# Kernel optimization log

Hardware: AMD Instinct MI355X
Metric: run time of the kernel (lower is better)

Reference implementation:

```python
import jax, jax.numpy as jnp
import numpy as np

CHUNK = 128
EPS = 1e-12


def causal_prod(q, k, v, chunk=CHUNK):
    """Chunk-parallel causal linear attention numerator and denominator.
    q,k: [B,H,S,D]; v: [B,H,S,E].
    Returns N: [B,H,S,E] = q_n . cumsum_{m<=n}(k_m v_m^T)
            D: [B,H,S]   = q_n . cumsum_{m<=n} k_m
    """
    B, H, S, D = q.shape
    E = v.shape[-1]
    nc = S // chunk
    # [nc, B, H, C, D]
    qc = q.reshape(B, H, nc, chunk, D).transpose(2, 0, 1, 3, 4)
    kc = k.reshape(B, H, nc, chunk, D).transpose(2, 0, 1, 3, 4)
    vc = v.reshape(B, H, nc, chunk, E).transpose(2, 0, 1, 3, 4)
    mask = jnp.tril(jnp.ones((chunk, chunk), dtype=bool))  # j <= i

    def step(carry, xs):
        S_state, Z_state = carry  # [B,H,D,E], [B,H,D]
        qb, kb, vb = xs           # [B,H,C,D], [B,H,C,D], [B,H,C,E]
        scores = jnp.einsum('bhid,bhjd->bhij', qb, kb)
        scores = jnp.where(mask, scores, 0.0)
        # intra-chunk causal part + inter-chunk state part
        Nb = jnp.einsum('bhij,bhje->bhie', scores, vb) \
             + jnp.einsum('bhid,bhde->bhie', qb, S_state)
        Db = scores.sum(-1) + jnp.einsum('bhid,bhd->bhi', qb, Z_state)
        S_state = S_state + jnp.einsum('bhjd,bhje->bhde', kb, vb)
        Z_state = Z_state + kb.sum(axis=2)
        return (S_state, Z_state), (Nb, Db)

    init = (jnp.zeros((B, H, D, E), q.dtype), jnp.zeros((B, H, D), q.dtype))
    _, (N, Dv) = jax.lax.scan(step, init, (qc, kc, vc))
    N = N.transpose(1, 2, 0, 3, 4).reshape(B, H, S, E)
    Dv = Dv.transpose(1, 2, 0, 3).reshape(B, H, S)
    return N, Dv


def setup_inputs() -> dict:
    key = jax.random.key(0)
    k0, k1, k2, k3, k4 = jax.random.split(key, 5)
    B, H, S, D = 2, 8, 4096, 64
    # feature-mapped q/k are positive (softmax random features) -> uniform
    q = jax.random.uniform(k0, (B, H, S, D), dtype=jnp.float32)
    k = jax.random.uniform(k1, (B, H, S, D), dtype=jnp.float32)
    q_rot = jax.random.uniform(k2, (B, H, S, D), dtype=jnp.float32)
    k_rot = jax.random.uniform(k3, (B, H, S, D), dtype=jnp.float32)
    v = jax.random.normal(k4, (B, H, S, D), dtype=jnp.float32)
    return {"q": q, "k": k, "q_rot": q_rot, "k_rot": k_rot, "v": v, "horizon": 512}


def reference(q, k, q_rot, k_rot, v, horizon):
    # causal_linear_attention with local=horizon, rotary branch active
    N1, D1 = causal_prod(q, k, v)
    N2, D2 = causal_prod(q_rot, k_rot, v)
    N = N1 + N2
    Dd = D1 + D2
    local = horizon
    # subtract contribution of keys older than the local window
    ql = q[:, :, local:]
    kl = k[:, :, :-local]
    vl = v[:, :, :-local]
    qrl = q_rot[:, :, local:]
    krl = k_rot[:, :, :-local]
    Ns1, Ds1 = causal_prod(ql, kl, vl)
    Ns2, Ds2 = causal_prod(qrl, krl, vl)
    N = N.at[:, :, local:].add(-(Ns1 + Ns2))
    Dd = Dd.at[:, :, local:].add(-(Ds1 + Ds2))
    out = N * (1.0 / (Dd + EPS))[..., None]
    return out
```

## Files before the change

kernel.cpp:

```cpp
#include <hip/hip_runtime.h>

#define S_LEN 4096
#define Dh 64
#define KC_TILE 16384
#define VT_TILE 8192

typedef __attribute__((ext_vector_type(8))) short bf16x8;
typedef __attribute__((ext_vector_type(4))) short bf16x4;
typedef __attribute__((ext_vector_type(4))) float f32x4;
typedef __attribute__((ext_vector_type(16))) float f32x16;
typedef __attribute__((ext_vector_type(4))) unsigned u32x4;

__device__ __forceinline__ short f2bf(float f) {
    union { float f; unsigned u; } c; c.f = f;
    unsigned u = c.u + 0x7FFFu + ((c.u >> 16) & 1u);
    return (short)(u >> 16);
}

__device__ __forceinline__ unsigned cvt_pk(float lo, float hi) {
    unsigned r;
    asm("v_cvt_pk_bf16_f32 %0, %1, %2" : "=v"(r) : "v"(lo), "v"(hi));
    return r;
}

__device__ __forceinline__ void pl32swap(unsigned& a, unsigned& b) {
    asm("v_permlane32_swap_b32 %0, %1" : "+v"(a), "+v"(b));
}

__global__ __launch_bounds__(256) void prepack2(
    const float* __restrict__ k, const float* __restrict__ kr,
    const float* __restrict__ v, char* __restrict__ ws,
    unsigned long long vt_base, int k_slots)
{
    const int t = blockIdx.x * 256 + threadIdx.x;
    if (t < k_slots) {
        const int bh = t >> 16;
        const int r = t & 65535;
        const int tile = r >> 10;
        const int s = r & 1023;
        const int l = s & 63;
        const int c = s >> 6;
        const int fs = c >> 1, half = c & 1;
        const int key = half * 32 + (l & 31);
        const int f0 = fs * 16 + (l >> 5) * 8;
        const size_t row = ((size_t)bh * S_LEN + tile * 64 + key) * Dh;
        const float* src = (f0 < 64) ? (k + row + f0) : (kr + row + f0 - 64);
        f32x4 a = *(const f32x4*)src;
        f32x4 b = *(const f32x4*)(src + 4);
        u32x4 w;
        w[0] = cvt_pk(a[0], a[1]); w[1] = cvt_pk(a[2], a[3]);
        w[2] = cvt_pk(b[0], b[1]); w[3] = cvt_pk(b[2], b[3]);
        *(u32x4*)(ws + (size_t)(bh * 64 + tile) * KC_TILE + s * 16) = w;
    } else {
        const int t2 = t - k_slots;
        const int bh = t2 >> 15;
        const int r = t2 & 32767;
        const int tile = r >> 9;
        const int s = r & 511;
        const int l = s & 63;
        const int c = s >> 6;
        const int kb = c >> 2, ks = (c >> 1) & 1, eh = c & 1;
        const int e = eh * 32 + (l & 31);
        const int key0 = kb * 32 + ks * 16 + (l >> 5) * 8;
        const float* src = v + ((size_t)bh * S_LEN + tile * 64 + key0) * Dh + e;
        float x0 = src[0],      x1 = src[Dh],     x2 = src[2 * Dh], x3 = src[3 * Dh];
        float x4 = src[4 * Dh], x5 = src[5 * Dh], x6 = src[6 * Dh], x7 = src[7 * Dh];
        u32x4 w;
        w[0] = cvt_pk(x0, x1); w[1] = cvt_pk(x2, x3);
        w[2] = cvt_pk(x4, x5); w[3] = cvt_pk(x6, x7);
        *(u32x4*)(ws + vt_base + (size_t)(bh * 64 + tile) * VT_TILE + s * 16) = w;
    }
}

__global__ __launch_bounds__(64, 2) void swin_attn4(
    const float* __restrict__ q, const float* __restrict__ qr,
    const char* __restrict__ ws, unsigned long long vt_base,
    const int* __restrict__ hor, float* __restrict__ out)
{
    const int W = hor[0];
    const int nwg = gridDim.x;
    const int cpx = nwg >> 3;
    const int bid = blockIdx.x;
    const int wg = (bid & 7) * cpx + (bid >> 3);
    const int bh = wg >> 7;
    const int q0 = (wg & 127) * 32;
    const size_t base = (size_t)bh * S_LEN * Dh;

    const int lane = threadIdx.x;
    const int hi = lane >> 5;
    const int l32 = lane & 31;

    __shared__ float sD[32];

    const int qg = q0 + l32;

    bf16x8 qf[8];
    {
        const float* qrow  = q  + base + (size_t)qg * Dh;
        const float* qrrow = qr + base + (size_t)qg * Dh;
        #pragma unroll
        for (int fs = 0; fs < 8; ++fs) {
            int feat = fs * 16 + hi * 8;
            const float* src = (feat < 64) ? (qrow + feat) : (qrrow + feat - 64);
            f32x4 a = *(const f32x4*)src;
            f32x4 b = *(const f32x4*)(src + 4);
            u32x4 w;
            w[0] = cvt_pk(a[0], a[1]); w[1] = cvt_pk(a[2], a[3]);
            w[2] = cvt_pk(b[0], b[1]); w[3] = cvt_pk(b[2], b[3]);
            qf[fs] = __builtin_bit_cast(bf16x8, w);
        }
    }

    f32x16 nacc0 = {};
    f32x16 nacc1 = {};
    float dsum = 0.f;

    const int lo_key = q0 - (W - 1);
    const int kt_lo = (lo_key <= 0) ? 0 : (lo_key >> 6);
    const int kt_hi = (q0 + 31) >> 6;

    const char* Kc = ws + (size_t)(bh << 6) * KC_TILE + lane * 16;
    const char* Vt = ws + vt_base + (size_t)(bh << 6) * VT_TILE + lane * 16;

    bf16x8 kf[16];
    bf16x8 vf[8];
    {
        const char* kp = Kc + (size_t)kt_lo * KC_TILE;
        const char* vp = Vt + (size_t)kt_lo * VT_TILE;
        #pragma unroll
        for (int c = 0; c < 16; ++c) kf[c] = *(const bf16x8*)(kp + c * 1024);
        #pragma unroll
        for (int c = 0; c < 8; ++c)  vf[c] = *(const bf16x8*)(vp + c * 1024);
    }

    for (int kt = kt_lo; kt <= kt_hi; ++kt) {
        const int k0 = kt << 6;
        const int ktn = (kt < kt_hi) ? kt + 1 : kt_hi;
        const bool dense = (k0 + 63 <= q0) && (k0 >= q0 + 32 - W);

        f32x16 sac0 = {};
        f32x16 sac1 = {};
        __builtin_amdgcn_s_setprio(1);
        #pragma unroll
        for (int fs = 0; fs < 8; ++fs) {
            sac0 = __builtin_amdgcn_mfma_f32_32x32x16_bf16(kf[fs * 2],     qf[fs], sac0, 0, 0, 0);
            sac1 = __builtin_amdgcn_mfma_f32_32x32x16_bf16(kf[fs * 2 + 1], qf[fs], sac1, 0, 0, 0);
        }
        __builtin_amdgcn_s_setprio(0);

        {
            const char* kp = Kc + (size_t)ktn * KC_TILE;
            #pragma unroll
            for (int c = 0; c < 16; ++c) kf[c] = *(const bf16x8*)(kp + c * 1024);
        }

        #pragma unroll
        for (int kb = 0; kb < 2; ++kb) {
            f32x16 s = kb ? sac1 : sac0;
            if (!dense) {
                #pragma unroll
                for (int r = 0; r < 16; ++r) {
                    int key = k0 + kb * 32 + (r & 3) + 8 * (r >> 2) + 4 * hi;
                    if ((unsigned)(qg - key) >= (unsigned)W) s[r] = 0.f;
                }
            }
            #pragma unroll
            for (int r = 0; r < 16; ++r) dsum += s[r];

            unsigned w0 = cvt_pk(s[0],  s[1]);
            unsigned w1 = cvt_pk(s[2],  s[3]);
            unsigned w2 = cvt_pk(s[4],  s[5]);
            unsigned w3 = cvt_pk(s[6],  s[7]);
            unsigned w4 = cvt_pk(s[8],  s[9]);
            unsigned w5 = cvt_pk(s[10], s[11]);
            unsigned w6 = cvt_pk(s[12], s[13]);
            unsigned w7 = cvt_pk(s[14], s[15]);
            pl32swap(w0, w2);
            pl32swap(w1, w3);
            pl32swap(w4, w6);
            pl32swap(w5, w7);
            u32x4 p0v = {w0, w1, w2, w3};
            u32x4 p1v = {w4, w5, w6, w7};
            bf16x8 pa0 = __builtin_bit_cast(bf16x8, p0v);
            bf16x8 pa1 = __builtin_bit_cast(bf16x8, p1v);

            __builtin_amdgcn_s_setprio(1);
            #pragma unroll
            for (int ks = 0; ks < 2; ++ks) {
                bf16x8 pa = ks ? pa1 : pa0;
                nacc0 = __builtin_amdgcn_mfma_f32_32x32x16_bf16(pa, vf[kb * 4 + ks * 2],     nacc0, 0, 0, 0);
                nacc1 = __builtin_amdgcn_mfma_f32_32x32x16_bf16(pa, vf[kb * 4 + ks * 2 + 1], nacc1, 0, 0, 0);
            }
            __builtin_amdgcn_s_setprio(0);
        }

        {
            const char* vp = Vt + (size_t)ktn * VT_TILE;
            #pragma unroll
            for (int c = 0; c < 8; ++c) vf[c] = *(const bf16x8*)(vp + c * 1024);
        }
    }

    unsigned da = __builtin_bit_cast(unsigned, dsum);
    unsigned db = da;
    pl32swap(da, db);
    float dfull = __builtin_bit_cast(float, da) + __builtin_bit_cast(float, db);
    float rcq = 1.0f / (dfull + 1e-12f);
    if (lane < 32) sD[l32] = rcq;
    __syncthreads();
    float rcv[16];
    #pragma unroll
    for (int r = 0; r < 16; ++r)
        rcv[r] = sD[(r & 3) + 8 * (r >> 2) + 4 * hi];

    #pragma unroll
    for (int r = 0; r < 16; ++r) {
        const int qrow = q0 + (r & 3) + 8 * (r >> 2) + 4 * hi;
        float* o = out + base + (size_t)qrow * Dh + l32;
        o[0]  = nacc0[r] * rcv[r];
        o[32] = nacc1[r] * rcv[r];
    }
}

__global__ __launch_bounds__(256, 2) void swin_attn_fb(
    const float* __restrict__ q, const float* __restrict__ k,
    const float* __restrict__ qr, const float* __restrict__ kr,
    const float* __restrict__ v, const int* __restrict__ hor,
    float* __restrict__ out)
{
    const int W = hor[0];
    const int q0 = blockIdx.x * 128;
    const int bh = blockIdx.y;
    const size_t base = (size_t)bh * S_LEN * Dh;

    const int tid = threadIdx.x;
    const int lane = tid & 63;
    const int wv = tid >> 6;
    const int g = lane >> 4;
    const int l16 = lane & 15;

    __shared__ __align__(16) char sK[64 * 256];
    __shared__ __align__(16) char sV[64 * 128];
    __shared__ __align__(16) char sS[4][32 * 128];

    bf16x8 qf[2][4];
    #pragma unroll
    for (int rb = 0; rb < 2; ++rb) {
        int qg = q0 + wv * 32 + rb * 16 + l16;
        const float* qrow  = q  + base + (size_t)qg * Dh;
        const float* qrrow = qr + base + (size_t)qg * Dh;
        #pragma unroll
        for (int fb = 0; fb < 4; ++fb) {
            int feat = fb * 32 + g * 8;
            const float* src = (feat < 64) ? (qrow + feat) : (qrrow + (feat - 64));
            f32x4 a = *(const f32x4*)src;
            f32x4 b = *(const f32x4*)(src + 4);
            bf16x8 fr;
            #pragma unroll
            for (int j = 0; j < 4; ++j) { fr[j] = f2bf(a[j]); fr[4 + j] = f2bf(b[j]); }
            qf[rb][fb] = fr;
        }
    }

    f32x4 nacc[2][4];
    f32x4 dacc[2];
    #pragma unroll
    for (int rb = 0; rb < 2; ++rb) {
        dacc[rb] = (f32x4){0.f, 0.f, 0.f, 0.f};
        #pragma unroll
        for (int eb = 0; eb < 4; ++eb) nacc[rb][eb] = (f32x4){0.f, 0.f, 0.f, 0.f};
    }
    bf16x8 ones;
    #pragma unroll
    for (int j = 0; j < 8; ++j) ones[j] = (short)0x3F80;

    const int lo_key = q0 - (W - 1);
    const int kt_lo = (lo_key <= 0) ? 0 : (lo_key >> 6);
    const int kt_hi = (q0 + 127) >> 6;

    for (int kt = kt_lo; kt <= kt_hi; ++kt) {
        const int k0 = kt << 6;
        __syncthreads();
        #pragma unroll
        for (int i = 0; i < 4; ++i) {
            int c = tid + 256 * i;
            int row = c >> 4;
            int f0 = (c & 15) * 8;
            const float* src = (f0 < 64) ? (k  + base + (size_t)(k0 + row) * Dh + f0)
                                         : (kr + base + (size_t)(k0 + row) * Dh + (f0 - 64));
            f32x4 a = *(const f32x4*)src;
            f32x4 b = *(const f32x4*)(src + 4);
            bf16x8 w8;
            #pragma unroll
            for (int j = 0; j < 4; ++j) { w8[j] = f2bf(a[j]); w8[4 + j] = f2bf(b[j]); }
            int off = row * 256 + ((f0 * 2) ^ ((row & 7) << 4));
            *(bf16x8*)(sK + off) = w8;
        }
        #pragma unroll
        for (int i = 0; i < 4; ++i) {
            int c = tid + 256 * i;
            int e = c & 63;
            int k4 = c >> 6;
            const float* src = v + base + (size_t)(k0 + k4 * 4) * Dh + e;
            bf16x4 w4;
            w4[0] = f2bf(src[0]); w4[1] = f2bf(src[Dh]);
            w4[2] = f2bf(src[2 * Dh]); w4[3] = f2bf(src[3 * Dh]);
            int off = e * 128 + ((k4 * 8) ^ ((e & 7) << 4));
            *(bf16x4*)(sV + off) = w4;
        }
        __syncthreads();

        const bool dense = (k0 + 63 <= q0) && (k0 >= q0 + 128 - W);
        #pragma unroll
        for (int kb = 0; kb < 4; ++kb) {
            bf16x8 kf[4];
            const int key = kb * 16 + l16;
            const int rowoff = key * 256;
            const int sw = (key & 7) << 4;
            #pragma unroll
            for (int fb = 0; fb < 4; ++fb)
                kf[fb] = *(const bf16x8*)(sK + rowoff + ((fb * 64 + g * 16) ^ sw));
            #pragma unroll
            for (int rb = 0; rb < 2; ++rb) {
                f32x4 s = {0.f, 0.f, 0.f, 0.f};
                #pragma unroll
                for (int fb = 0; fb < 4; ++fb)
                    s = __builtin_amdgcn_mfma_f32_16x16x32_bf16(qf[rb][fb], kf[fb], s, 0, 0, 0);
                const int qrow0 = rb * 16 + g * 4;
                const int qg0 = q0 + wv * 32 + qrow0;
                const int mg = k0 + kb * 16 + l16;
                if (!dense) {
                    #pragma unroll
                    for (int r = 0; r < 4; ++r) {
                        unsigned d = (unsigned)(qg0 + r - mg);
                        if (d >= (unsigned)W) s[r] = 0.f;
                    }
                }
                #pragma unroll
                for (int r = 0; r < 4; ++r) {
                    int row = qrow0 + r;
                    int off = row * 128 + (((kb * 16 + l16) * 2) ^ ((row & 7) << 4));
                    *(short*)(sS[wv] + off) = f2bf(s[r]);
                }
            }
        }
        #pragma unroll
        for (int kb2 = 0; kb2 < 2; ++kb2) {
            bf16x8 af[2];
            #pragma unroll
            for (int rb = 0; rb < 2; ++rb) {
                int row = rb * 16 + l16;
                int off = row * 128 + ((kb2 * 64 + g * 16) ^ ((row & 7) << 4));
                af[rb] = *(const bf16x8*)(sS[wv] + off);
            }
            #pragma unroll
            for (int rb = 0; rb < 2; ++rb)
                dacc[rb] = __builtin_amdgcn_mfma_f32_16x16x32_bf16(af[rb], ones, dacc[rb], 0, 0, 0);
            #pragma unroll
            for (int eb = 0; eb < 4; ++eb) {
                int e = eb * 16 + l16;
                int off = e * 128 + ((kb2 * 64 + g * 16) ^ ((e & 7) << 4));
                bf16x8 bfr = *(const bf16x8*)(sV + off);
                #pragma unroll
                for (int rb = 0; rb < 2; ++rb)
                    nacc[rb][eb] = __builtin_amdgcn_mfma_f32_16x16x32_bf16(af[rb], bfr, nacc[rb][eb], 0, 0, 0);
            }
        }
    }

    #pragma unroll
    for (int rb = 0; rb < 2; ++rb) {
        f32x4 rc;
        #pragma unroll
        for (int r = 0; r < 4; ++r) rc[r] = 1.0f / (dacc[rb][r] + 1e-12f);
        const int qg0 = q0 + wv * 32 + rb * 16 + g * 4;
        #pragma unroll
        for (int eb = 0; eb < 4; ++eb) {
            #pragma unroll
            for (int r = 0; r < 4; ++r) {
                out[base + (size_t)(qg0 + r) * Dh + eb * 16 + l16] = nacc[rb][eb][r] * rc[r];
            }
        }
    }
}

extern "C" void kernel_launch(void* const* d_in, const int* in_sizes, int n_in,
                              void* d_out, int out_size, void* d_ws, size_t ws_size,
                              hipStream_t stream) {
    const float* q  = (const float*)d_in[0];
    const float* k  = (const float*)d_in[1];
    const float* qr = (const float*)d_in[2];
    const float* kr = (const float*)d_in[3];
    const float* v  = (const float*)d_in[4];
    const int* hor  = (const int*)d_in[5];
    float* out = (float*)d_out;

    const int BH = in_sizes[0] / (S_LEN * Dh);
    const unsigned long long vt_base = (unsigned long long)BH * 64 * KC_TILE;
    const unsigned long long ws_need = (unsigned long long)BH * 64 * (KC_TILE + VT_TILE);
    const int k_slots = BH * 65536;

    if (ws_size >= ws_need) {
        const int total_slots = BH * (65536 + 32768);
        hipLaunchKernelGGL(prepack2, dim3(total_slots / 256), dim3(256), 0, stream,
                           k, kr, v, (char*)d_ws, vt_base, k_slots);
        hipLaunchKernelGGL(swin_attn4, dim3(BH * 128), dim3(64), 0, stream,
                           q, qr, (const char*)d_ws, vt_base, hor, out);
    } else {
        hipLaunchKernelGGL(swin_attn_fb, dim3(S_LEN / 128, BH), dim3(256), 0, stream,
                           q, k, qr, kr, v, hor, out);
    }
}
```

Measured before the change: 42.31 us.

## Iterate key tiles at 32-key granularity to trim window edges and registers

The key loop now walks half-tiles of 32 keys instead of 64, so the windowed range starts and ends tighter around each 32-query block and skips partly empty half-tiles at the edges. The smaller prefetched K/V register arrays lower register pressure, and launch bounds are raised to allow three waves per SIMD. In exchange there are more loop iterations, each with its own masking, bf16 conversion and lane-swap overhead, and less MFMA work per iteration for hiding prefetch latency.

```diff
diff --git a/kernel.cpp b/kernel.cpp
--- a/kernel.cpp
+++ b/kernel.cpp
@@ -72,7 +72,7 @@
     }
 }
 
-__global__ __launch_bounds__(64, 2) void swin_attn4(
+__global__ __launch_bounds__(64, 3) void swin_attn5(
     const float* __restrict__ q, const float* __restrict__ qr,
     const char* __restrict__ ws, unsigned long long vt_base,
     const int* __restrict__ hor, float* __restrict__ out)
@@ -115,91 +115,77 @@
     f32x16 nacc1 = {};
     float dsum = 0.f;
 
-    const int lo_key = q0 - (W - 1);
-    const int kt_lo = (lo_key <= 0) ? 0 : (lo_key >> 6);
-    const int kt_hi = (q0 + 31) >> 6;
+    const int lo_q = q0 - W + 1;
+    const int h_lo = (lo_q <= 0) ? 0 : (lo_q >> 5);
+    const int h_hi = (q0 + 31) >> 5;
 
     const char* Kc = ws + (size_t)(bh << 6) * KC_TILE + lane * 16;
     const char* Vt = ws + vt_base + (size_t)(bh << 6) * VT_TILE + lane * 16;
 
-    bf16x8 kf[16];
-    bf16x8 vf[8];
-    {
-        const char* kp = Kc + (size_t)kt_lo * KC_TILE;
-        const char* vp = Vt + (size_t)kt_lo * VT_TILE;
-        #pragma unroll
-        for (int c = 0; c < 16; ++c) kf[c] = *(const bf16x8*)(kp + c * 1024);
-        #pragma unroll
-        for (int c = 0; c < 8; ++c)  vf[c] = *(const bf16x8*)(vp + c * 1024);
-    }
-
-    for (int kt = kt_lo; kt <= kt_hi; ++kt) {
-        const int k0 = kt << 6;
-        const int ktn = (kt < kt_hi) ? kt + 1 : kt_hi;
-        const bool dense = (k0 + 63 <= q0) && (k0 >= q0 + 32 - W);
-
-        f32x16 sac0 = {};
-        f32x16 sac1 = {};
+#define KADDR(H, FS) (Kc + (size_t)((H) >> 1) * KC_TILE + ((((FS) << 1) + ((H) & 1)) << 10))
+#define VADDR(H, C)  (Vt + (size_t)((H) >> 1) * VT_TILE + (((((H) & 1) << 2) + (C)) << 10))
+
+    bf16x8 kf[8];
+    bf16x8 vf[4];
+    #pragma unroll
+    for (int fs = 0; fs < 8; ++fs) kf[fs] = *(const bf16x8*)KADDR(h_lo, fs);
+    #pragma unroll
+    for (int c = 0; c < 4; ++c)    vf[c] = *(const bf16x8*)VADDR(h_lo, c);
+
+    for (int h = h_lo; h <= h_hi; ++h) {
+        const int hn = (h < h_hi) ? h + 1 : h;
+        const int k0h = h << 5;
+
+        f32x16 sac = {};
         __builtin_amdgcn_s_setprio(1);
         #pragma unroll
-        for (int fs = 0; fs < 8; ++fs) {
-            sac0 = __builtin_amdgcn_mfma_f32_32x32x16_bf16(kf[fs * 2],     qf[fs], sac0, 0, 0, 0);
-            sac1 = __builtin_amdgcn_mfma_f32_32x32x16_bf16(kf[fs * 2 + 1], qf[fs], sac1, 0, 0, 0);
-        }
+        for (int fs = 0; fs < 8; ++fs)
+            sac = __builtin_amdgcn_mfma_f32_32x32x16_bf16(kf[fs], qf[fs], sac, 0, 0, 0);
         __builtin_amdgcn_s_setprio(0);
 
-        {
-            const char* kp = Kc + (size_t)ktn * KC_TILE;
-            #pragma unroll
-            for (int c = 0; c < 16; ++c) kf[c] = *(const bf16x8*)(kp + c * 1024);
-        }
-
-        #pragma unroll
-        for (int kb = 0; kb < 2; ++kb) {
-            f32x16 s = kb ? sac1 : sac0;
-            if (!dense) {
-                #pragma unroll
-                for (int r = 0; r < 16; ++r) {
-                    int key = k0 + kb * 32 + (r & 3) + 8 * (r >> 2) + 4 * hi;
-                    if ((unsigned)(qg - key) >= (unsigned)W) s[r] = 0.f;
-                }
-            }
-            #pragma unroll
-            for (int r = 0; r < 16; ++r) dsum += s[r];
-
-            unsigned w0 = cvt_pk(s[0],  s[1]);
-            unsigned w1 = cvt_pk(s[2],  s[3]);
-            unsigned w2 = cvt_pk(s[4],  s[5]);
-            unsigned w3 = cvt_pk(s[6],  s[7]);
-            unsigned w4 = cvt_pk(s[8],  s[9]);
-            unsigned w5 = cvt_pk(s[10], s[11]);
-            unsigned w6 = cvt_pk(s[12], s[13]);
-            unsigned w7 = cvt_pk(s[14], s[15]);
-            pl32swap(w0, w2);
-            pl32swap(w1, w3);
-            pl32swap(w4, w6);
-            pl32swap(w5, w7);
-            u32x4 p0v = {w0, w1, w2, w3};
-            u32x4 p1v = {w4, w5, w6, w7};
-            bf16x8 pa0 = __builtin_bit_cast(bf16x8, p0v);
-            bf16x8 pa1 = __builtin_bit_cast(bf16x8, p1v);
-
-            __builtin_amdgcn_s_setprio(1);
-            #pragma unroll
-            for (int ks = 0; ks < 2; ++ks) {
-                bf16x8 pa = ks ? pa1 : pa0;
-                nacc0 = __builtin_amdgcn_mfma_f32_32x32x16_bf16(pa, vf[kb * 4 + ks * 2],     nacc0, 0, 0, 0);
-                nacc1 = __builtin_amdgcn_mfma_f32_32x32x16_bf16(pa, vf[kb * 4 + ks * 2 + 1], nacc1, 0, 0, 0);
-            }
-            __builtin_amdgcn_s_setprio(0);
-        }
-
-        {
-            const char* vp = Vt + (size_t)ktn * VT_TILE;
-            #pragma unroll
-            for (int c = 0; c < 8; ++c) vf[c] = *(const bf16x8*)(vp + c * 1024);
-        }
-    }
+        #pragma unroll
+        for (int fs = 0; fs < 8; ++fs) kf[fs] = *(const bf16x8*)KADDR(hn, fs);
+
+        const bool dense = (k0h + 31 <= q0) && (k0h >= q0 + 32 - W);
+        if (!dense) {
+            #pragma unroll
+            for (int r = 0; r < 16; ++r) {
+                int key = k0h + (r & 3) + 8 * (r >> 2) + 4 * hi;
+                if ((unsigned)(qg - key) >= (unsigned)W) sac[r] = 0.f;
+            }
+        }
+        #pragma unroll
+        for (int r = 0; r < 16; ++r) dsum += sac[r];
+
+        unsigned w0 = cvt_pk(sac[0],  sac[1]);
+        unsigned w1 = cvt_pk(sac[2],  sac[3]);
+        unsigned w2 = cvt_pk(sac[4],  sac[5]);
+        unsigned w3 = cvt_pk(sac[6],  sac[7]);
+        unsigned w4 = cvt_pk(sac[8],  sac[9]);
+        unsigned w5 = cvt_pk(sac[10], sac[11]);
+        unsigned w6 = cvt_pk(sac[12], sac[13]);
+        unsigned w7 = cvt_pk(sac[14], sac[15]);
+        pl32swap(w0, w2);
+        pl32swap(w1, w3);
+        pl32swap(w4, w6);
+        pl32swap(w5, w7);
+        u32x4 p0v = {w0, w1, w2, w3};
+        u32x4 p1v = {w4, w5, w6, w7};
+        bf16x8 pa0 = __builtin_bit_cast(bf16x8, p0v);
+        bf16x8 pa1 = __builtin_bit_cast(bf16x8, p1v);
+
+        __builtin_amdgcn_s_setprio(1);
+        nacc0 = __builtin_amdgcn_mfma_f32_32x32x16_bf16(pa0, vf[0], nacc0, 0, 0, 0);
+        nacc1 = __builtin_amdgcn_mfma_f32_32x32x16_bf16(pa0, vf[1], nacc1, 0, 0, 0);
+        nacc0 = __builtin_amdgcn_mfma_f32_32x32x16_bf16(pa1, vf[2], nacc0, 0, 0, 0);
+        nacc1 = __builtin_amdgcn_mfma_f32_32x32x16_bf16(pa1, vf[3], nacc1, 0, 0, 0);
+        __builtin_amdgcn_s_setprio(0);
+
+        #pragma unroll
+        for (int c = 0; c < 4; ++c) vf[c] = *(const bf16x8*)VADDR(hn, c);
+    }
+#undef KADDR
+#undef VADDR
 
     unsigned da = __builtin_bit_cast(unsigned, dsum);
     unsigned db = da;
@@ -404,7 +390,7 @@
         const int total_slots = BH * (65536 + 32768);
         hipLaunchKernelGGL(prepack2, dim3(total_slots / 256), dim3(256), 0, stream,
                            k, kr, v, (char*)d_ws, vt_base, k_slots);
-        hipLaunchKernelGGL(swin_attn4, dim3(BH * 128), dim3(64), 0, stream,
+        hipLaunchKernelGGL(swin_attn5, dim3(BH * 128), dim3(64), 0, stream,
                            q, qr, (const char*)d_ws, vt_base, hor, out);
     } else {
         hipLaunchKernelGGL(swin_attn_fb, dim3(S_LEN / 128, BH), dim3(256), 0, stream,
```

New measurement: 42.91 us. About the same (+1.4%).
